# Kernel tuning notes

Measured on AMD Instinct MI355X. Metric: run time of the kernel, lower is better.

## Reference

```python
import jax, jax.numpy as jnp
import numpy as np

B, S, HID = 2, 1024, 2048
N_HEADS, N_KV, HEAD_DIM = 32, 4, 128
BLOCK, MAX_BLOCKS = 32, 128
EPS = 1e-6
ROPE_THETA = 1e6


def _rmsnorm(x, w):
    # per-head RMSNorm over head_dim (Qwen3MoeRMSNorm)
    var = jnp.mean(x * x, axis=-1, keepdims=True)
    return x * jax.lax.rsqrt(var + EPS) * w


def _rotate_half(x):
    h = x.shape[-1] // 2
    return jnp.concatenate([-x[..., h:], x[..., :h]], axis=-1)


def setup_inputs() -> dict:
    key = jax.random.key(0)
    ks = jax.random.split(key, 8)
    hidden_states = jax.random.normal(ks[0], (B, S, HID), dtype=jnp.float32)
    wq = jax.random.normal(ks[1], (N_HEADS * HEAD_DIM, HID), dtype=jnp.float32) * 0.02
    wk = jax.random.normal(ks[2], (N_KV * HEAD_DIM, HID), dtype=jnp.float32) * 0.02
    wv = jax.random.normal(ks[3], (N_KV * HEAD_DIM, HID), dtype=jnp.float32) * 0.02
    wo = jax.random.normal(ks[4], (HID, N_HEADS * HEAD_DIM), dtype=jnp.float32) * 0.02
    q_norm_w = 1.0 + 0.01 * jax.random.normal(ks[5], (HEAD_DIM,), dtype=jnp.float32)
    k_norm_w = 1.0 + 0.01 * jax.random.normal(ks[6], (HEAD_DIM,), dtype=jnp.float32)
    # RoPE tables (rotate-half / llama convention)
    inv_freq = 1.0 / (ROPE_THETA ** (jnp.arange(0, HEAD_DIM, 2, dtype=jnp.float32) / HEAD_DIM))
    t = jnp.arange(S, dtype=jnp.float32)
    freqs = jnp.outer(t, inv_freq)  # [S, HEAD_DIM/2]
    emb = jnp.concatenate([freqs, freqs], axis=-1)  # [S, HEAD_DIM]
    cos, sin = jnp.cos(emb), jnp.sin(emb)
    # page table: B sequences x (S/BLOCK) blocks, distinct block ids
    page_table = jnp.arange(B * (S // BLOCK), dtype=jnp.int32).reshape(B, S // BLOCK)
    return {"hidden_states": hidden_states, "wq": wq, "wk": wk, "wv": wv, "wo": wo,
            "q_norm_w": q_norm_w, "k_norm_w": k_norm_w, "cos": cos, "sin": sin,
            "page_table": page_table}


def reference(hidden_states, wq, wk, wv, wo, q_norm_w, k_norm_w, cos, sin, page_table):
    b, s, _ = hidden_states.shape
    # fused QKV projection (math-equivalent to the concatenated qkv_proj_weight)
    q = (hidden_states @ wq.T).reshape(b, s, N_HEADS, HEAD_DIM)
    k = (hidden_states @ wk.T).reshape(b, s, N_KV, HEAD_DIM)
    v = (hidden_states @ wv.T).reshape(b, s, N_KV, HEAD_DIM)
    # per-head RMSNorm then RoPE
    q = _rmsnorm(q, q_norm_w)
    k = _rmsnorm(k, k_norm_w)
    c = cos[None, :, None, :]
    sn = sin[None, :, None, :]
    q = q * c + _rotate_half(q) * sn
    k = k * c + _rotate_half(k) * sn
    # paged KV-cache fill: [B, nblk, BLOCK, kvh, hd] -> cache[block_id, kvh, BLOCK, hd]
    nblk = s // BLOCK
    k_blk = k.reshape(b, nblk, BLOCK, N_KV, HEAD_DIM).transpose(0, 1, 3, 2, 4).reshape(-1, N_KV, BLOCK, HEAD_DIM)
    v_blk = v.reshape(b, nblk, BLOCK, N_KV, HEAD_DIM).transpose(0, 1, 3, 2, 4).reshape(-1, N_KV, BLOCK, HEAD_DIM)
    flat_pt = page_table.reshape(-1)
    cache_k = jnp.zeros((MAX_BLOCKS, N_KV, BLOCK, HEAD_DIM), dtype=k.dtype).at[flat_pt].set(k_blk)
    cache_v = jnp.zeros((MAX_BLOCKS, N_KV, BLOCK, HEAD_DIM), dtype=v.dtype).at[flat_pt].set(v_blk)
    # GQA: repeat kv heads (num_key_value_groups = 8)
    groups = N_HEADS // N_KV
    k_rep = jnp.repeat(k, groups, axis=2)  # [b, s, N_HEADS, hd]
    v_rep = jnp.repeat(v, groups, axis=2)
    # causal SDPA, scaling = head_dim ** -0.5
    scale = HEAD_DIM ** -0.5
    scores = jnp.einsum('bqhd,bkhd->bhqk', q, k_rep) * scale
    causal = jnp.tril(jnp.ones((s, s), dtype=bool))
    scores = jnp.where(causal[None, None], scores, jnp.finfo(scores.dtype).min)
    probs = jax.nn.softmax(scores, axis=-1)
    attn = jnp.einsum('bhqk,bkhd->bqhd', probs, v_rep).reshape(b, s, N_HEADS * HEAD_DIM)
    out = attn @ wo.T  # [b, s, HID]
    return out, cache_k, cache_v
```

## Files before the change

### kernel.cpp

```cpp
#include <hip/hip_runtime.h>
#include <hip/hip_bf16.h>


typedef __attribute__((ext_vector_type(8))) __bf16 bf16x8;
typedef __attribute__((ext_vector_type(4))) __bf16 bf16x4;
typedef __attribute__((ext_vector_type(4))) float f32x4;

__device__ __forceinline__ void gload16(const void* g, void* l) {
    __builtin_amdgcn_global_load_lds((const __attribute__((address_space(1))) void*)g,
                                     (__attribute__((address_space(3))) void*)l, 16, 0, 0);
}

__global__ __launch_bounds__(256) void cvt5(const float* __restrict__ s0, const float* __restrict__ s1,
                                            const float* __restrict__ s2, const float* __restrict__ s3,
                                            const float* __restrict__ s4,
                                            __bf16* __restrict__ d0, __bf16* __restrict__ d1,
                                            __bf16* __restrict__ d2, __bf16* __restrict__ d3,
                                            __bf16* __restrict__ d4) {
    const int b = blockIdx.x;
    const float* src; __bf16* dst; int off;
    if (b < 2048)      { src = s0; dst = d0; off = b; }
    else if (b < 6144) { src = s1; dst = d1; off = b - 2048; }
    else if (b < 6656) { src = s2; dst = d2; off = b - 6144; }
    else if (b < 7168) { src = s3; dst = d3; off = b - 6656; }
    else               { src = s4; dst = d4; off = b - 7168; }
#pragma unroll
    for (int u = 0; u < 2; ++u) {
        const int i = off * 512 + u * 256 + threadIdx.x;
        float4 v = reinterpret_cast<const float4*>(src)[i];
        bf16x4 o = {(__bf16)v.x, (__bf16)v.y, (__bf16)v.z, (__bf16)v.w};
        reinterpret_cast<bf16x4*>(dst)[i] = o;
    }
}

__global__ __launch_bounds__(256) void reduce_add(float* __restrict__ o,
                                                  const float* __restrict__ p, int n4) {
    int i = blockIdx.x * 256 + threadIdx.x;
    int stride = gridDim.x * 256;
    for (; i < n4; i += stride) {
        float4 a = reinterpret_cast<float4*>(o)[i];
        float4 b = reinterpret_cast<const float4*>(p)[i];
        a.x += b.x; a.y += b.y; a.z += b.z; a.w += b.w;
        reinterpret_cast<float4*>(o)[i] = a;
    }
}

template <int NF, int OUT_BF16>
__global__ __launch_bounds__(512, 2) void gemm4p(const __bf16* __restrict__ A,
                                                 const __bf16* __restrict__ B,
                                                 void* __restrict__ C0,
                                                 void* __restrict__ C1,
                                                 const int M, const int N, const int K,
                                                 const int nTiles, const int nbn,
                                                 const int klen) {
    __shared__ __bf16 Asm[2 * 128 * 64];
    __shared__ __bf16 Bsm[2 * NF * 64 * 64];
    const int tid = threadIdx.x, lane = tid & 63, wave = tid >> 6;
    const int wm = wave >> 2, wn = wave & 3;
    const int lrow = lane & 15, lkg = lane >> 4;
    const int rsw = lrow & 7;
    const int bid = blockIdx.x;
    const int kz = bid / nTiles, tile = bid % nTiles;
    const int tswz = (tile & 7) * (nTiles >> 3) + (tile >> 3);
    const int bm = tswz / nbn, bn = tswz % nbn;
    const int brow = bm * 128, bcol = bn * (NF * 64);
    const int kbeg = kz * klen;
    const int row0 = tid >> 3;
    const int scol_sw = ((tid & 7) ^ (row0 & 7)) * 8;
    const __bf16* gA = A + (size_t)(brow + row0) * K + kbeg + scol_sw;
    const __bf16* gB = B + (size_t)(bcol + row0) * K + kbeg + scol_sw;
    const int slot0 = (lkg ^ rsw) * 8;
    const int slot1 = ((4 + lkg) ^ rsw) * 8;
    const int nt = klen / 64;
    constexpr int UPT = NF + 2;

    f32x4 acc[4][NF] = {};

    int su_t = 0, su_w = 0;
    auto stage1 = [&]() {
        if (su_t < nt) {
            const size_t ko = (size_t)su_t * 64;
            if (su_w < 2)
                gload16(gA + (size_t)(su_w * 64) * K + ko,
                        Asm + (su_t & 1) * 8192 + su_w * 4096 + tid * 8);
            else
                gload16(gB + (size_t)((su_w - 2) * 64) * K + ko,
                        Bsm + (su_t & 1) * (NF * 4096) + (su_w - 2) * 4096 + tid * 8);
        }
        if (++su_w == UPT) { su_w = 0; ++su_t; }
    };

    for (int u = 0; u < 2 * UPT; ++u) stage1();
    if constexpr (NF == 5) asm volatile("s_waitcnt vmcnt(7)" ::: "memory");
    else                   asm volatile("s_waitcnt vmcnt(6)" ::: "memory");
    __builtin_amdgcn_s_barrier();

    for (int t = 0; t < nt; ++t) {
        const __bf16* As = Asm + (t & 1) * 8192;
        const __bf16* Bs = Bsm + (t & 1) * (NF * 4096);
        bf16x8 ar[4], br[NF];
#pragma unroll
        for (int mi = 0; mi < 4; ++mi)
            ar[mi] = *reinterpret_cast<const bf16x8*>(&As[(wm * 64 + mi * 16 + lrow) * 64 + slot0]);
#pragma unroll
        for (int nf = 0; nf < NF; ++nf)
            br[nf] = *reinterpret_cast<const bf16x8*>(&Bs[(wn * (NF * 16) + nf * 16 + lrow) * 64 + slot0]);
        asm volatile("s_waitcnt lgkmcnt(0)" ::: "memory");
        __builtin_amdgcn_sched_barrier(0);
        __builtin_amdgcn_s_setprio(1);
#pragma unroll
        for (int mi = 0; mi < 4; ++mi)
#pragma unroll
            for (int nf = 0; nf < NF; ++nf)
                acc[mi][nf] = __builtin_amdgcn_mfma_f32_16x16x32_bf16(ar[mi], br[nf], acc[mi][nf], 0, 0, 0);
        __builtin_amdgcn_s_setprio(0);
        __builtin_amdgcn_s_barrier();
#pragma unroll
        for (int mi = 0; mi < 4; ++mi)
            ar[mi] = *reinterpret_cast<const bf16x8*>(&As[(wm * 64 + mi * 16 + lrow) * 64 + slot1]);
#pragma unroll
        for (int nf = 0; nf < NF; ++nf)
            br[nf] = *reinterpret_cast<const bf16x8*>(&Bs[(wn * (NF * 16) + nf * 16 + lrow) * 64 + slot1]);
        asm volatile("s_waitcnt lgkmcnt(0)" ::: "memory");
#pragma unroll
        for (int u = 0; u < UPT; ++u) stage1();
        __builtin_amdgcn_sched_barrier(0);
        __builtin_amdgcn_s_setprio(1);
#pragma unroll
        for (int mi = 0; mi < 4; ++mi)
#pragma unroll
            for (int nf = 0; nf < NF; ++nf)
                acc[mi][nf] = __builtin_amdgcn_mfma_f32_16x16x32_bf16(ar[mi], br[nf], acc[mi][nf], 0, 0, 0);
        __builtin_amdgcn_s_setprio(0);
        if (t + 2 < nt) {
            if constexpr (NF == 5) asm volatile("s_waitcnt vmcnt(7)" ::: "memory");
            else                   asm volatile("s_waitcnt vmcnt(6)" ::: "memory");
        } else {
            asm volatile("s_waitcnt vmcnt(0)" ::: "memory");
        }
        __builtin_amdgcn_s_barrier();
    }

    void* C = (kz == 0) ? C0 : C1;
#pragma unroll
    for (int mi = 0; mi < 4; ++mi)
#pragma unroll
        for (int nf = 0; nf < NF; ++nf)
#pragma unroll
            for (int j = 0; j < 4; ++j) {
                const size_t r = brow + wm * 64 + mi * 16 + lkg * 4 + j;
                const size_t c = bcol + wn * (NF * 16) + nf * 16 + lrow;
                if (OUT_BF16)
                    ((__bf16*)C)[r * N + c] = (__bf16)acc[mi][nf][j];
                else
                    ((float*)C)[r * N + c] = acc[mi][nf][j];
            }
}

__global__ __launch_bounds__(256) void norm_rope_cache(
    __bf16* __restrict__ qkv, const float* __restrict__ cosT, const float* __restrict__ sinT,
    const float* __restrict__ qw, const float* __restrict__ kw,
    const int* __restrict__ ptab, float* __restrict__ cacheK, float* __restrict__ cacheV) {
    const int t = blockIdx.x;
    const int b = t >> 10, s = t & 1023;
    const int wave = threadIdx.x >> 6, lane = threadIdx.x & 63;
    __bf16* row = qkv + (size_t)t * 5120;
    const float c = cosT[s * 128 + lane];
    const float sn = sinT[s * 128 + lane];
    const int page = ptab[b * 32 + (s >> 5)];
    const int so = s & 31;
    const float wq0 = qw[lane], wq1 = qw[lane + 64];
#pragma unroll
    for (int i = 0; i < 8; ++i) {
        const int h = wave * 8 + i;
        float x0 = (float)row[h * 128 + lane];
        float x1 = (float)row[h * 128 + 64 + lane];
        float ss = x0 * x0 + x1 * x1;
        for (int off = 32; off; off >>= 1) ss += __shfl_xor(ss, off);
        const float rs = rsqrtf(ss * (1.0f / 128.0f) + 1e-6f);
        const float y0 = x0 * rs * wq0, y1 = x1 * rs * wq1;
        row[h * 128 + lane]      = (__bf16)(y0 * c - y1 * sn);
        row[h * 128 + 64 + lane] = (__bf16)(y1 * c + y0 * sn);
    }
    {
        const int h = wave;
        float x0 = (float)row[4096 + h * 128 + lane];
        float x1 = (float)row[4096 + h * 128 + 64 + lane];
        float ss = x0 * x0 + x1 * x1;
        for (int off = 32; off; off >>= 1) ss += __shfl_xor(ss, off);
        const float rs = rsqrtf(ss * (1.0f / 128.0f) + 1e-6f);
        const float y0 = x0 * rs * kw[lane], y1 = x1 * rs * kw[lane + 64];
        const float o0 = y0 * c - y1 * sn, o1 = y1 * c + y0 * sn;
        row[4096 + h * 128 + lane]      = (__bf16)o0;
        row[4096 + h * 128 + 64 + lane] = (__bf16)o1;
        float* ck = cacheK + (((size_t)page * 4 + h) * 32 + so) * 128;
        ck[lane] = o0; ck[lane + 64] = o1;
        const float v0 = (float)row[4608 + h * 128 + lane];
        const float v1 = (float)row[4608 + h * 128 + 64 + lane];
        float* cv = cacheV + (((size_t)page * 4 + h) * 32 + so) * 128;
        cv[lane] = v0; cv[lane + 64] = v1;
    }
}

__global__ __launch_bounds__(512, 2) void attn_fwd(const __bf16* __restrict__ qkv,
                                                   __bf16* __restrict__ out) {
    __shared__ __bf16 Ks[2][128 * 128];
    __shared__ __bf16 Vs[128 * 128];
    __shared__ __bf16 Ps[8][2][16 * 64];
    const int bid = blockIdx.x;
    const int qa = bid >> 3;
    const int g = bid & 7;
    const int kvg = g & 3, b = g >> 2;
    const int qbig = 63 - qa;
    const int tid = threadIdx.x, wave = tid >> 6, lane = tid & 63;
    const int lrow = lane & 15, lkg = lane >> 4;
    const int h = kvg * 8 + wave;
    const size_t base = (size_t)b * 1024 * 5120;
    const int kofs = 4096 + kvg * 128, vofs = 4608 + kvg * 128;
    const int ntA = qa / 8 + 1, nt = qbig / 8 + 1;
    const int lastA = qa >> 2, lastB = qbig >> 2;
    const int qposA = qa * 16 + lrow, qposB = qbig * 16 + lrow;
    const int rsw = lrow & 7;
    constexpr float QS = 0.08838834764831845f * 1.4426950408889634f;
    constexpr float SUB = 20.0f;

    bf16x8 aqA[4], aqB[4];
#pragma unroll
    for (int kc = 0; kc < 4; ++kc) {
        bf16x8 ta = *reinterpret_cast<const bf16x8*>(
            &qkv[base + (size_t)(qa * 16 + lrow) * 5120 + h * 128 + kc * 32 + lkg * 8]);
        bf16x8 tb = *reinterpret_cast<const bf16x8*>(
            &qkv[base + (size_t)(qbig * 16 + lrow) * 5120 + h * 128 + kc * 32 + lkg * 8]);
#pragma unroll
        for (int i = 0; i < 8; ++i) {
            ta[i] = (__bf16)((float)ta[i] * QS);
            tb[i] = (__bf16)((float)tb[i] * QS);
        }
        aqA[kc] = ta; aqB[kc] = tb;
    }

    f32x4 accA[8] = {}, accB[8] = {};
    float lA = 0.f, lB = 0.f;
    __bf16* PwA = &Ps[wave][0][0];
    __bf16* PwB = &Ps[wave][1][0];

    auto stageK = [&](int t, int buf) {
        const int kv0 = (t < nt) ? t * 128 : 0;
#pragma unroll
        for (int c = 0; c < 4; ++c) {
            const int chunk = c * 8 + wave;
            const int row = chunk * 4 + (lane >> 4);
            const int gslot = (lane & 15) ^ (row & 7);
            gload16(&qkv[base + (size_t)(kv0 + row) * 5120 + kofs + gslot * 8],
                    &Ks[buf][chunk * 512]);
        }
    };
    auto loadV = [&](int t, uint4 (&vr)[4]) {
        const int kv0 = (t < nt) ? t * 128 : 0;
#pragma unroll
        for (int r = 0; r < 4; ++r) {
            const int kv = 2 * lane + (r & 1);
            const int d0 = wave * 16 + (r >> 1) * 8;
            vr[r] = *reinterpret_cast<const uint4*>(
                &qkv[base + (size_t)(kv0 + kv) * 5120 + vofs + d0]);
        }
    };
    auto writeV = [&](uint4 (&vr)[4]) {
        const int slot = lane >> 2;
        const int klo = (2 * lane) & 7;
#pragma unroll
        for (int hh = 0; hh < 2; ++hh) {
            const unsigned short* e0 = reinterpret_cast<const unsigned short*>(&vr[2 * hh]);
            const unsigned short* e1 = reinterpret_cast<const unsigned short*>(&vr[2 * hh + 1]);
#pragma unroll
            for (int j = 0; j < 8; ++j) {
                const int d = wave * 16 + hh * 8 + j;
                const unsigned val = (unsigned)e0[j] | ((unsigned)e1[j] << 16);
                *reinterpret_cast<unsigned*>(
                    &Vs[d * 128 + ((slot ^ (d & 7)) << 3) + klo]) = val;
            }
        }
    };

    auto smax = [&](f32x4 (&st)[4], float& l_lane, int qpos, int kv0, bool maskit, __bf16* Pw) {
#pragma unroll
        for (int f = 0; f < 4; ++f) {
            bf16x4 pb;
#pragma unroll
            for (int j = 0; j < 4; ++j) {
                float x = st[f][j];
                if (maskit) {
                    const int kvpos = kv0 + f * 16 + lkg * 4 + j;
                    if (kvpos > qpos) x = -1e30f;
                }
                const float p = exp2f(x - SUB);
                l_lane += p;
                pb[j] = (__bf16)p;
            }
            const int slot = (f * 2 + (lkg >> 1)) ^ rsw;
            *reinterpret_cast<bf16x4*>(&Pw[lrow * 64 + slot * 8 + (lkg & 1) * 4]) = pb;
        }
    };

    auto pvH = [&](f32x4 (&acc)[8], int hf, __bf16* Pw) {
#pragma unroll
        for (int kk = 0; kk < 2; ++kk) {
            const int pslot = ((kk * 4 + lkg) ^ rsw) << 3;
            bf16x8 ap = *reinterpret_cast<const bf16x8*>(&Pw[lrow * 64 + pslot]);
#pragma unroll
            for (int f = 0; f < 8; ++f) {
                bf16x8 bv = *reinterpret_cast<const bf16x8*>(
                    &Vs[(f * 16 + lrow) * 128 + hf * 64 + pslot]);
                acc[f] = __builtin_amdgcn_mfma_f32_16x16x32_bf16(ap, bv, acc[f], 0, 0, 0);
            }
        }
    };

    auto body = [&](int t, uint4 (&vcur)[4], uint4 (&vnext)[4]) {
        const int kbuf = t & 1;
        __builtin_amdgcn_s_barrier();
        asm volatile("" ::: "memory");
        loadV(t + 1, vnext);
        stageK(t + 1, kbuf ^ 1);
        asm volatile("s_waitcnt vmcnt(8)" ::: "memory");
        writeV(vcur);
        asm volatile("s_waitcnt lgkmcnt(0)" ::: "memory");
        __builtin_amdgcn_s_barrier();
        asm volatile("" ::: "memory");

        const bool doA = t < ntA;
#pragma unroll
        for (int hf = 0; hf < 2; ++hf) {
            const int kh = 2 * t + hf;
            const bool actA = doA && (kh <= lastA);
            const bool actB = kh <= lastB;
            if (!actB && !actA) continue;
            f32x4 stA[4] = {}, stB[4] = {};
#pragma unroll
            for (int kc = 0; kc < 4; ++kc)
#pragma unroll
                for (int f = 0; f < 4; ++f) {
                    bf16x8 ak = *reinterpret_cast<const bf16x8*>(
                        &Ks[kbuf][(hf * 64 + f * 16 + lrow) * 128 + (((kc * 4 + lkg) ^ rsw) << 3)]);
                    if (actB)
                        stB[f] = __builtin_amdgcn_mfma_f32_16x16x32_bf16(ak, aqB[kc], stB[f], 0, 0, 0);
                    if (actA)
                        stA[f] = __builtin_amdgcn_mfma_f32_16x16x32_bf16(ak, aqA[kc], stA[f], 0, 0, 0);
                }
            const int kv0 = t * 128 + hf * 64;
            if (actA) {
                smax(stA, lA, qposA, kv0, kh == lastA, PwA);
                pvH(accA, hf, PwA);
            }
            if (actB) {
                smax(stB, lB, qposB, kv0, kh == lastB, PwB);
                pvH(accB, hf, PwB);
            }
        }
    };

    uint4 vrA[4], vrB[4];
    loadV(0, vrA);
    stageK(0, 0);
    for (int t = 0; t < nt; t += 2) {
        body(t, vrA, vrB);
        if (t + 1 < nt) body(t + 1, vrB, vrA);
    }
    asm volatile("s_waitcnt vmcnt(0)" ::: "memory");

    lA += __shfl_xor(lA, 16); lA += __shfl_xor(lA, 32);
    lB += __shfl_xor(lB, 16); lB += __shfl_xor(lB, 32);
    float linvA[4], linvB[4];
#pragma unroll
    for (int j = 0; j < 4; ++j) {
        linvA[j] = 1.0f / __shfl(lA, lkg * 4 + j);
        linvB[j] = 1.0f / __shfl(lB, lkg * 4 + j);
    }
#pragma unroll
    for (int f = 0; f < 8; ++f)
#pragma unroll
        for (int j = 0; j < 4; ++j) {
            out[((size_t)b * 1024 + qa * 16 + lkg * 4 + j) * 4096 + h * 128 + f * 16 + lrow] =
                (__bf16)(accA[f][j] * linvA[j]);
            out[((size_t)b * 1024 + qbig * 16 + lkg * 4 + j) * 4096 + h * 128 + f * 16 + lrow] =
                (__bf16)(accB[f][j] * linvB[j]);
        }
}

extern "C" void kernel_launch(void* const* d_in, const int* in_sizes, int n_in,
                              void* d_out, int out_size, void* d_ws, size_t ws_size,
                              hipStream_t stream) {
    const float* hidden = (const float*)d_in[0];
    const float* wq = (const float*)d_in[1];
    const float* wk = (const float*)d_in[2];
    const float* wv = (const float*)d_in[3];
    const float* wo = (const float*)d_in[4];
    const float* qnw = (const float*)d_in[5];
    const float* knw = (const float*)d_in[6];
    const float* cosT = (const float*)d_in[7];
    const float* sinT = (const float*)d_in[8];
    const int* ptab = (const int*)d_in[9];

    float* outp = (float*)d_out;
    float* cacheK = outp + 4194304;
    float* cacheV = cacheK + 2097152;

    char* ws = (char*)d_ws;
    __bf16* hbf    = (__bf16*)ws;
    __bf16* w1bf   = (__bf16*)(ws + 8388608);
    __bf16* wobf   = (__bf16*)(ws + 29360128);
    __bf16* qkvbf  = (__bf16*)(ws + 46137344);
    __bf16* attnbf = (__bf16*)ws;
    float*  opart  = (float*)(ws + 46137344);

    cvt5<<<11264, 256, 0, stream>>>(hidden, wq, wk, wv, wo,
                                    hbf, w1bf, w1bf + (size_t)4096 * 2048,
                                    w1bf + (size_t)4608 * 2048, wobf);

    gemm4p<5, 1><<<256, 512, 0, stream>>>(hbf, w1bf, qkvbf, nullptr,
                                          2048, 5120, 2048, 256, 16, 2048);

    hipMemsetAsync(cacheK + 1048576, 0, (size_t)1048576 * 4, stream);
    hipMemsetAsync(cacheV + 1048576, 0, (size_t)1048576 * 4, stream);
    norm_rope_cache<<<2048, 256, 0, stream>>>(qkvbf, cosT, sinT, qnw, knw, ptab, cacheK, cacheV);

    attn_fwd<<<256, 512, 0, stream>>>(qkvbf, attnbf);

    gemm4p<4, 0><<<256, 512, 0, stream>>>(attnbf, wobf, outp, opart,
                                          2048, 2048, 4096, 128, 8, 2048);
    reduce_add<<<2048, 256, 0, stream>>>(outp, opart, 4194304 / 4);
}
```

Measured before the change: 190.5 us.

## Read K fragments directly from global in attention, widen fp32-to-bf16 conversion

The attention kernel drops the double-buffered LDS staging of K tiles and has each wave load its K MFMA operands straight from global memory. This frees LDS and removes the async K copy, and launch bounds are relaxed to one block per SM. The V writes are reordered ahead of the next V prefetch with a full vmcnt wait. Separately, the conversion kernel now handles 8 elements per thread with half the blocks. The trade-off is that K reads now expose global latency and redundant cache traffic across waves, and V prefetch overlap is reduced.

```diff
diff --git a/kernel.cpp b/kernel.cpp
--- a/kernel.cpp
+++ b/kernel.cpp
@@ -19,17 +19,19 @@
                                             __bf16* __restrict__ d4) {
     const int b = blockIdx.x;
     const float* src; __bf16* dst; int off;
-    if (b < 2048)      { src = s0; dst = d0; off = b; }
-    else if (b < 6144) { src = s1; dst = d1; off = b - 2048; }
-    else if (b < 6656) { src = s2; dst = d2; off = b - 6144; }
-    else if (b < 7168) { src = s3; dst = d3; off = b - 6656; }
-    else               { src = s4; dst = d4; off = b - 7168; }
+    if (b < 1024)      { src = s0; dst = d0; off = b; }
+    else if (b < 3072) { src = s1; dst = d1; off = b - 1024; }
+    else if (b < 3328) { src = s2; dst = d2; off = b - 3072; }
+    else if (b < 3584) { src = s3; dst = d3; off = b - 3328; }
+    else               { src = s4; dst = d4; off = b - 3584; }
 #pragma unroll
     for (int u = 0; u < 2; ++u) {
         const int i = off * 512 + u * 256 + threadIdx.x;
-        float4 v = reinterpret_cast<const float4*>(src)[i];
-        bf16x4 o = {(__bf16)v.x, (__bf16)v.y, (__bf16)v.z, (__bf16)v.w};
-        reinterpret_cast<bf16x4*>(dst)[i] = o;
+        float4 v0 = reinterpret_cast<const float4*>(src)[2 * i];
+        float4 v1 = reinterpret_cast<const float4*>(src)[2 * i + 1];
+        bf16x8 o = {(__bf16)v0.x, (__bf16)v0.y, (__bf16)v0.z, (__bf16)v0.w,
+                    (__bf16)v1.x, (__bf16)v1.y, (__bf16)v1.z, (__bf16)v1.w};
+        reinterpret_cast<bf16x8*>(dst)[i] = o;
     }
 }
 
@@ -202,9 +204,8 @@
     }
 }
 
-__global__ __launch_bounds__(512, 2) void attn_fwd(const __bf16* __restrict__ qkv,
+__global__ __launch_bounds__(512, 1) void attn_fwd(const __bf16* __restrict__ qkv,
                                                    __bf16* __restrict__ out) {
-    __shared__ __bf16 Ks[2][128 * 128];
     __shared__ __bf16 Vs[128 * 128];
     __shared__ __bf16 Ps[8][2][16 * 64];
     const int bid = blockIdx.x;
@@ -223,6 +224,7 @@
     const int rsw = lrow & 7;
     constexpr float QS = 0.08838834764831845f * 1.4426950408889634f;
     constexpr float SUB = 20.0f;
+    const __bf16* gK = qkv + base + kofs;
 
     bf16x8 aqA[4], aqB[4];
 #pragma unroll
@@ -244,17 +246,6 @@
     __bf16* PwA = &Ps[wave][0][0];
     __bf16* PwB = &Ps[wave][1][0];
 
-    auto stageK = [&](int t, int buf) {
-        const int kv0 = (t < nt) ? t * 128 : 0;
-#pragma unroll
-        for (int c = 0; c < 4; ++c) {
-            const int chunk = c * 8 + wave;
-            const int row = chunk * 4 + (lane >> 4);
-            const int gslot = (lane & 15) ^ (row & 7);
-            gload16(&qkv[base + (size_t)(kv0 + row) * 5120 + kofs + gslot * 8],
-                    &Ks[buf][chunk * 512]);
-        }
-    };
     auto loadV = [&](int t, uint4 (&vr)[4]) {
         const int kv0 = (t < nt) ? t * 128 : 0;
 #pragma unroll
@@ -317,13 +308,10 @@
     };
 
     auto body = [&](int t, uint4 (&vcur)[4], uint4 (&vnext)[4]) {
-        const int kbuf = t & 1;
         __builtin_amdgcn_s_barrier();
-        asm volatile("" ::: "memory");
+        asm volatile("s_waitcnt vmcnt(0)" ::: "memory");
+        writeV(vcur);
         loadV(t + 1, vnext);
-        stageK(t + 1, kbuf ^ 1);
-        asm volatile("s_waitcnt vmcnt(8)" ::: "memory");
-        writeV(vcur);
         asm volatile("s_waitcnt lgkmcnt(0)" ::: "memory");
         __builtin_amdgcn_s_barrier();
         asm volatile("" ::: "memory");
@@ -335,25 +323,25 @@
             const bool actA = doA && (kh <= lastA);
             const bool actB = kh <= lastB;
             if (!actB && !actA) continue;
+            const int kvr0 = t * 128 + hf * 64;
             f32x4 stA[4] = {}, stB[4] = {};
 #pragma unroll
             for (int kc = 0; kc < 4; ++kc)
 #pragma unroll
                 for (int f = 0; f < 4; ++f) {
                     bf16x8 ak = *reinterpret_cast<const bf16x8*>(
-                        &Ks[kbuf][(hf * 64 + f * 16 + lrow) * 128 + (((kc * 4 + lkg) ^ rsw) << 3)]);
+                        &gK[(size_t)(kvr0 + f * 16 + lrow) * 5120 + kc * 32 + lkg * 8]);
                     if (actB)
                         stB[f] = __builtin_amdgcn_mfma_f32_16x16x32_bf16(ak, aqB[kc], stB[f], 0, 0, 0);
                     if (actA)
                         stA[f] = __builtin_amdgcn_mfma_f32_16x16x32_bf16(ak, aqA[kc], stA[f], 0, 0, 0);
                 }
-            const int kv0 = t * 128 + hf * 64;
             if (actA) {
-                smax(stA, lA, qposA, kv0, kh == lastA, PwA);
+                smax(stA, lA, qposA, kvr0, kh == lastA, PwA);
                 pvH(accA, hf, PwA);
             }
             if (actB) {
-                smax(stB, lB, qposB, kv0, kh == lastB, PwB);
+                smax(stB, lB, qposB, kvr0, kh == lastB, PwB);
                 pvH(accB, hf, PwB);
             }
         }
@@ -361,7 +349,6 @@
 
     uint4 vrA[4], vrB[4];
     loadV(0, vrA);
-    stageK(0, 0);
     for (int t = 0; t < nt; t += 2) {
         body(t, vrA, vrB);
         if (t + 1 < nt) body(t + 1, vrB, vrA);
@@ -413,9 +400,9 @@
     __bf16* attnbf = (__bf16*)ws;
     float*  opart  = (float*)(ws + 46137344);
 
-    cvt5<<<11264, 256, 0, stream>>>(hidden, wq, wk, wv, wo,
-                                    hbf, w1bf, w1bf + (size_t)4096 * 2048,
-                                    w1bf + (size_t)4608 * 2048, wobf);
+    cvt5<<<5632, 256, 0, stream>>>(hidden, wq, wk, wv, wo,
+                                   hbf, w1bf, w1bf + (size_t)4096 * 2048,
+                                   w1bf + (size_t)4608 * 2048, wobf);
 
     gemm4p<5, 1><<<256, 512, 0, stream>>>(hbf, w1bf, qkvbf, nullptr,
                                           2048, 5120, 2048, 256, 16, 2048);
```

After: 240.7 us. 1.26x slower.

## Replace split-K partial buffer and reduce kernel with atomic adds; widen fp32-to-bf16 conversion

Applied to the files above, without the earlier changes.

The output projection's split-K now accumulates straight into a zeroed output buffer with float atomic adds. This removes the separate fp32 partial buffer and the reduce_add kernel, at the cost of a memset of the output and atomic traffic on every element. The conversion kernel also handles 8 elements per thread with 16-byte bf16 stores, halving its grid. Atomic ordering makes the summation order, and so the exact low bits of the result, nondeterministic.

```diff
diff --git a/kernel.cpp b/kernel.cpp
--- a/kernel.cpp
+++ b/kernel.cpp
@@ -19,29 +19,19 @@
                                             __bf16* __restrict__ d4) {
     const int b = blockIdx.x;
     const float* src; __bf16* dst; int off;
-    if (b < 2048)      { src = s0; dst = d0; off = b; }
-    else if (b < 6144) { src = s1; dst = d1; off = b - 2048; }
-    else if (b < 6656) { src = s2; dst = d2; off = b - 6144; }
-    else if (b < 7168) { src = s3; dst = d3; off = b - 6656; }
-    else               { src = s4; dst = d4; off = b - 7168; }
+    if (b < 1024)      { src = s0; dst = d0; off = b; }
+    else if (b < 3072) { src = s1; dst = d1; off = b - 1024; }
+    else if (b < 3328) { src = s2; dst = d2; off = b - 3072; }
+    else if (b < 3584) { src = s3; dst = d3; off = b - 3328; }
+    else               { src = s4; dst = d4; off = b - 3584; }
 #pragma unroll
     for (int u = 0; u < 2; ++u) {
         const int i = off * 512 + u * 256 + threadIdx.x;
-        float4 v = reinterpret_cast<const float4*>(src)[i];
-        bf16x4 o = {(__bf16)v.x, (__bf16)v.y, (__bf16)v.z, (__bf16)v.w};
-        reinterpret_cast<bf16x4*>(dst)[i] = o;
-    }
-}
-
-__global__ __launch_bounds__(256) void reduce_add(float* __restrict__ o,
-                                                  const float* __restrict__ p, int n4) {
-    int i = blockIdx.x * 256 + threadIdx.x;
-    int stride = gridDim.x * 256;
-    for (; i < n4; i += stride) {
-        float4 a = reinterpret_cast<float4*>(o)[i];
-        float4 b = reinterpret_cast<const float4*>(p)[i];
-        a.x += b.x; a.y += b.y; a.z += b.z; a.w += b.w;
-        reinterpret_cast<float4*>(o)[i] = a;
+        float4 v0 = reinterpret_cast<const float4*>(src)[2 * i];
+        float4 v1 = reinterpret_cast<const float4*>(src)[2 * i + 1];
+        bf16x8 o = {(__bf16)v0.x, (__bf16)v0.y, (__bf16)v0.z, (__bf16)v0.w,
+                    (__bf16)v1.x, (__bf16)v1.y, (__bf16)v1.z, (__bf16)v1.w};
+        reinterpret_cast<bf16x8*>(dst)[i] = o;
     }
 }
 
@@ -141,7 +131,6 @@
         __builtin_amdgcn_s_barrier();
     }
 
-    void* C = (kz == 0) ? C0 : C1;
 #pragma unroll
     for (int mi = 0; mi < 4; ++mi)
 #pragma unroll
@@ -151,10 +140,11 @@
                 const size_t r = brow + wm * 64 + mi * 16 + lkg * 4 + j;
                 const size_t c = bcol + wn * (NF * 16) + nf * 16 + lrow;
                 if (OUT_BF16)
-                    ((__bf16*)C)[r * N + c] = (__bf16)acc[mi][nf][j];
+                    ((__bf16*)C0)[r * N + c] = (__bf16)acc[mi][nf][j];
                 else
-                    ((float*)C)[r * N + c] = acc[mi][nf][j];
-            }
+                    unsafeAtomicAdd(&((float*)C0)[r * N + c], acc[mi][nf][j]);
+            }
+    (void)C1;
 }
 
 __global__ __launch_bounds__(256) void norm_rope_cache(
@@ -411,11 +401,12 @@
     __bf16* wobf   = (__bf16*)(ws + 29360128);
     __bf16* qkvbf  = (__bf16*)(ws + 46137344);
     __bf16* attnbf = (__bf16*)ws;
-    float*  opart  = (float*)(ws + 46137344);
-
-    cvt5<<<11264, 256, 0, stream>>>(hidden, wq, wk, wv, wo,
-                                    hbf, w1bf, w1bf + (size_t)4096 * 2048,
-                                    w1bf + (size_t)4608 * 2048, wobf);
+
+    hipMemsetAsync(outp, 0, (size_t)4194304 * 4, stream);
+
+    cvt5<<<5632, 256, 0, stream>>>(hidden, wq, wk, wv, wo,
+                                   hbf, w1bf, w1bf + (size_t)4096 * 2048,
+                                   w1bf + (size_t)4608 * 2048, wobf);
 
     gemm4p<5, 1><<<256, 512, 0, stream>>>(hbf, w1bf, qkvbf, nullptr,
                                           2048, 5120, 2048, 256, 16, 2048);
@@ -426,7 +417,6 @@
 
     attn_fwd<<<256, 512, 0, stream>>>(qkvbf, attnbf);
 
-    gemm4p<4, 0><<<256, 512, 0, stream>>>(attnbf, wobf, outp, opart,
+    gemm4p<4, 0><<<256, 512, 0, stream>>>(attnbf, wobf, outp, nullptr,
                                           2048, 2048, 4096, 128, 8, 2048);
-    reduce_add<<<2048, 256, 0, stream>>>(outp, opart, 4194304 / 4);
-}
+}
```

Result: slower. 206.5 us (+8.4%).
